# Optimization experiments

Hardware: AMD Instinct MI355X
Metric: run time of the kernel (lower is better)

The kernel has to match this reference:

```python
import jax, jax.numpy as jnp
import numpy as np


def setup_inputs() -> dict:
    key = jax.random.key(0)
    ks = jax.random.split(key, 5)
    B, S, D, H, K = 2, 2048, 1024, 16, 64
    std = 0.02
    return {
        "x": jax.random.normal(ks[0], (B, S, D), dtype=jnp.float32),
        "W_Q": jax.random.normal(ks[1], (H, D, K), dtype=jnp.float32) * std,
        "W_K": jax.random.normal(ks[2], (H, D, K), dtype=jnp.float32) * std,
        "W_V": jax.random.normal(ks[3], (H, D, K), dtype=jnp.float32) * std,
        "W_O": jax.random.normal(ks[4], (H, K, D), dtype=jnp.float32) * std,
        "b_Q": jnp.zeros((H, K), dtype=jnp.float32),
        "b_K": jnp.zeros((H, K), dtype=jnp.float32),
        "b_V": jnp.zeros((H, K), dtype=jnp.float32),
        "b_O": jnp.zeros((D,), dtype=jnp.float32),
    }


def reference(x, W_Q, W_K, W_V, W_O, b_Q, b_K, b_V, b_O):
    # x: (B, S, D); W_*: (H, D, K); W_O: (H, K, D)
    S = x.shape[1]
    d_head = W_Q.shape[-1]
    q = jnp.einsum('bpd,hdk->bphk', x, W_Q) + b_Q
    k = jnp.einsum('bpd,hdk->bphk', x, W_K) + b_K
    v = jnp.einsum('bpd,hdk->bphk', x, W_V) + b_V
    scores = jnp.einsum('bphk,bqhk->bhpq', q, k) / jnp.sqrt(jnp.float32(d_head))
    # causal mask: positions q > p (strict upper triangle) are masked
    causal = jnp.tril(jnp.ones((S, S), dtype=bool))
    scores = jnp.where(causal, scores, jnp.float32(-jnp.inf))
    pattern = jax.nn.softmax(scores, axis=-1)
    z = jnp.einsum('bhpq,bqhk->bphk', pattern, v)
    out = jnp.einsum('bphk,hkd->bpd', z, W_O) + b_O
    return out
```

## Files before the change

### kernel.cpp

```cpp
#include <hip/hip_runtime.h>

typedef unsigned short u16;
typedef __attribute__((ext_vector_type(4))) float f32x4;
typedef __attribute__((ext_vector_type(8))) short s16x8;
typedef __attribute__((ext_vector_type(4))) unsigned short u16x4;
typedef __attribute__((ext_vector_type(2))) unsigned int u32x2;

#define S_ 2048
#define D_ 1024
#define H_ 16
#define KH 64
#define M_ 4096
#define BH_ 32

__device__ __forceinline__ float bf2f(u16 v) {
    union { unsigned int u; float f; } x; x.u = ((unsigned int)v) << 16; return x.f;
}
__device__ __forceinline__ u16 f2bf(float f) {
    union { float ff; unsigned int u; } x; x.ff = f;
    unsigned int r = x.u + 0x7fffu + ((x.u >> 16) & 1u);
    return (u16)(r >> 16);
}
__device__ __forceinline__ unsigned int cvt_pk_bf16(float lo, float hi) {
    unsigned int d;
    asm("v_cvt_pk_bf16_f32 %0, %1, %2" : "=v"(d) : "v"(lo), "v"(hi));
    return d;
}

__global__ void kcvt_x(const float* __restrict__ x, u16* __restrict__ xb) {
    const int i = (blockIdx.x * 256 + threadIdx.x) * 4;
    const float4 v = *(const float4*)&x[i];
    u16x4 o;
    o.x = f2bf(v.x); o.y = f2bf(v.y); o.z = f2bf(v.z); o.w = f2bf(v.w);
    *(u16x4*)&xb[i] = o;
}

__global__ void ktrans_w(const float* __restrict__ WQ, const float* __restrict__ WK,
                         const float* __restrict__ WV, const float* __restrict__ WO,
                         u16* __restrict__ wt) {
    __shared__ u16 tile[64][65];
    const int mat = blockIdx.z;
    const float* src = (mat == 0) ? WQ : (mat == 1) ? WK : (mat == 2) ? WV : WO;
    u16* dst = wt + (size_t)mat * 1048576;
    const int a0 = blockIdx.x * 64, b0 = blockIdx.y * 64;
    const int t = threadIdx.x;
    const int bl = t & 63, ar = t >> 6;
    #pragma unroll
    for (int i = 0; i < 16; ++i) {
        int a = a0 + i * 4 + ar, b = b0 + bl;
        size_t sa = (mat < 3) ? (((size_t)(b >> 6)) << 16) + ((size_t)a << 6) + (b & 63)
                              : (size_t)a * 1024 + b;
        tile[i * 4 + ar][bl] = f2bf(src[sa]);
    }
    __syncthreads();
    #pragma unroll
    for (int i = 0; i < 16; ++i) {
        int bl2 = i * 4 + ar;
        dst[(size_t)(b0 + bl2) * 1024 + a0 + bl] = tile[bl][bl2];
    }
}

__global__ void ktrans_v(const u16* __restrict__ V, u16* __restrict__ Vt) {
    __shared__ u16 tile[64][65];
    const int bh = blockIdx.y;
    const int s0 = blockIdx.x * 64;
    const u16* src = V + (size_t)bh * S_ * KH;
    u16* dst = Vt + (size_t)bh * S_ * KH;
    const int t = threadIdx.x, kl = t & 63, sr = t >> 6;
    #pragma unroll
    for (int i = 0; i < 16; ++i)
        tile[i * 4 + sr][kl] = src[(size_t)(s0 + i * 4 + sr) * KH + kl];
    __syncthreads();
    #pragma unroll
    for (int i = 0; i < 16; ++i) {
        int k = i * 4 + sr;
        dst[(size_t)k * S_ + s0 + kl] = tile[kl][k];
    }
}

template <int MODE>
__global__ __launch_bounds__(256)
void kgemm(const u16* __restrict__ A, const u16* __restrict__ Wt,
           const float* __restrict__ b0p, const float* __restrict__ b1p,
           const float* __restrict__ b2p,
           u16* __restrict__ o0, u16* __restrict__ o1, u16* __restrict__ o2,
           float* __restrict__ fo) {
    __shared__ u16 As[2][128 * 32];
    __shared__ u16 Bs[2][128 * 32];
    const int t = threadIdx.x;
    const int l = t & 63, w = t >> 6;
    const int lq = l & 15, lg = l >> 4;
    const int wr = w >> 1, wc = w & 1;
    const int m0 = blockIdx.x * 128;
    const int n0 = blockIdx.y * 128;

    const u16* Bt;
    const float* bias;
    u16* out = nullptr;
    if constexpr (MODE == 0) {
        const int z = blockIdx.z;
        Bt = Wt + (size_t)z * 1048576;
        bias = (z == 0) ? b0p : (z == 1) ? b1p : b2p;
        out = (z == 0) ? o0 : (z == 1) ? o1 : o2;
    } else {
        Bt = Wt; bias = b0p;
    }

    f32x4 acc[4][4] = {};

    auto stage = [&](int kt, int buf) {
        #pragma unroll
        for (int i = 0; i < 2; ++i) {
            int idx = t + i * 256;
            int row = idx >> 2, cc = idx & 3;
            const u16* ga = A + (size_t)(m0 + row) * 1024 + kt * 32 + cc * 8;
            const u16* gb = Bt + (size_t)(n0 + row) * 1024 + kt * 32 + cc * 8;
            __builtin_amdgcn_global_load_lds(
                (const __attribute__((address_space(1))) unsigned int*)ga,
                (__attribute__((address_space(3))) unsigned int*)(&As[buf][idx * 8]),
                16, 0, 0);
            __builtin_amdgcn_global_load_lds(
                (const __attribute__((address_space(1))) unsigned int*)gb,
                (__attribute__((address_space(3))) unsigned int*)(&Bs[buf][idx * 8]),
                16, 0, 0);
        }
    };

    stage(0, 0);
    __syncthreads();
    for (int kt = 0; kt < 32; ++kt) {
        const int cur = kt & 1;
        if (kt + 1 < 32) stage(kt + 1, cur ^ 1);
        s16x8 af[4], bf[4];
        #pragma unroll
        for (int m = 0; m < 4; ++m)
            af[m] = *(const s16x8*)&As[cur][(wr * 64 + m * 16 + lq) * 32 + lg * 8];
        #pragma unroll
        for (int n = 0; n < 4; ++n)
            bf[n] = *(const s16x8*)&Bs[cur][(wc * 64 + n * 16 + lq) * 32 + lg * 8];
        #pragma unroll
        for (int m = 0; m < 4; ++m)
            #pragma unroll
            for (int n = 0; n < 4; ++n)
                acc[m][n] = __builtin_amdgcn_mfma_f32_16x16x32_bf16(
                    af[m], bf[n], acc[m][n], 0, 0, 0);
        __syncthreads();
    }

    #pragma unroll
    for (int n = 0; n < 4; ++n) {
        const int gcol = n0 + wc * 64 + n * 16 + lq;
        const float bv = bias[gcol];
        #pragma unroll
        for (int m = 0; m < 4; ++m) {
            const int growb = m0 + wr * 64 + m * 16 + lg * 4;
            #pragma unroll
            for (int r = 0; r < 4; ++r) {
                const float v = acc[m][n][r] + bv;
                const int grow = growb + r;
                if constexpr (MODE == 0) {
                    const int b = grow >> 11, s = grow & 2047;
                    const int h = gcol >> 6, kk = gcol & 63;
                    out[(((size_t)(b * H_ + h)) * S_ + s) * KH + kk] = f2bf(v);
                } else {
                    fo[(size_t)grow * 1024 + gcol] = v;
                }
            }
        }
    }
}

__global__ __launch_bounds__(256)
void kattn(const u16* __restrict__ Q, const u16* __restrict__ K,
           const u16* __restrict__ Vt, u16* __restrict__ Z) {
    __shared__ u16 Ks[2][64 * 64];
    __shared__ u16 Vs[2][64 * 64];
    __shared__ u16 Pl[4][16 * 72];
    const int t = threadIdx.x, l = t & 63, w = t >> 6;
    const int lq = l & 15, lg = l >> 4;
    const int bh = blockIdx.y, pair = blockIdx.x;
    const size_t base = (size_t)bh * (S_ * KH);
    const u16* Qb = Q + base;
    const u16* Kb = K + base;
    const u16* Vb = Vt + base;
    const int b = bh >> 4, h = bh & 15;
    u16* Pw = &Pl[w][0];

    const int c0 = ((lg ^ (lq & 7)) * 8);
    const int c1 = c0 ^ 32;
    const float NINF = -__builtin_inff();

    auto stage = [&](int k0, int buf) {
        #pragma unroll
        for (int i = 0; i < 2; ++i) {
            const int idx = t + i * 256;
            const int row = idx >> 3;
            const int cg = (idx & 7) ^ (row & 7);
            __builtin_amdgcn_global_load_lds(
                (const __attribute__((address_space(1))) unsigned int*)
                    (Kb + (size_t)(k0 + row) * KH + cg * 8),
                (__attribute__((address_space(3))) unsigned int*)(&Ks[buf][idx * 8]),
                16, 0, 0);
            __builtin_amdgcn_global_load_lds(
                (const __attribute__((address_space(1))) unsigned int*)
                    (Vb + (size_t)row * S_ + k0 + cg * 8),
                (__attribute__((address_space(3))) unsigned int*)(&Vs[buf][idx * 8]),
                16, 0, 0);
        }
    };

    const float SCL = 0.18033688011112042f;

    #pragma unroll 1
    for (int ph = 0; ph < 2; ++ph) {
        const int qt = ph ? (31 - pair) : pair;
        const int nt = qt + 1;
        const int qs = qt * 64 + w * 16;
        const int lim = w * 16 + lq;

        const s16x8 qf0 = *(const s16x8*)&Qb[(size_t)(qs + lq) * KH + lg * 8];
        const s16x8 qf1 = *(const s16x8*)&Qb[(size_t)(qs + lq) * KH + 32 + lg * 8];

        float mrow = NINF;
        float lrow = 0.f;
        f32x4 zacc[4] = {};

        stage(0, 0);
        __syncthreads();

        for (int kt = 0; kt < nt; ++kt) {
            const int buf = kt & 1;
            if (kt + 1 < nt) stage((kt + 1) * 64, buf ^ 1);

            f32x4 sf[4] = {};
            __builtin_amdgcn_s_setprio(1);
            #pragma unroll
            for (int kf = 0; kf < 4; ++kf) {
                const int row = kf * 16 + lq;
                const s16x8 ka = *(const s16x8*)&Ks[buf][row * 64 + c0];
                const s16x8 kb = *(const s16x8*)&Ks[buf][row * 64 + c1];
                sf[kf] = __builtin_amdgcn_mfma_f32_16x16x32_bf16(ka, qf0, sf[kf], 0, 0, 0);
                sf[kf] = __builtin_amdgcn_mfma_f32_16x16x32_bf16(kb, qf1, sf[kf], 0, 0, 0);
            }
            __builtin_amdgcn_s_setprio(0);

            float p[4][4];
            const bool diag = (kt == qt);
            #pragma unroll
            for (int kf = 0; kf < 4; ++kf)
                #pragma unroll
                for (int r = 0; r < 4; ++r) {
                    float v = sf[kf][r] * SCL;
                    if (diag && (kf * 16 + lg * 4 + r) > lim) v = NINF;
                    p[kf][r] = v;
                }

            float mk[4];
            #pragma unroll
            for (int kf = 0; kf < 4; ++kf)
                mk[kf] = fmaxf(fmaxf(p[kf][0], p[kf][1]), fmaxf(p[kf][2], p[kf][3]));
            float tmax = fmaxf(fmaxf(mk[0], mk[1]), fmaxf(mk[2], mk[3]));
            tmax = fmaxf(tmax, __shfl_xor(tmax, 16));
            tmax = fmaxf(tmax, __shfl_xor(tmax, 32));

            float alpha = 1.f;
            if (!__all(tmax <= mrow + 8.f)) {
                const float nm = fmaxf(mrow, tmax);
                alpha = exp2f(mrow - nm);
                mrow = nm;
                float alp[4];
                #pragma unroll
                for (int r = 0; r < 4; ++r)
                    alp[r] = __shfl(alpha, lg * 4 + r);
                #pragma unroll
                for (int nf = 0; nf < 4; ++nf)
                    #pragma unroll
                    for (int r = 0; r < 4; ++r)
                        zacc[nf][r] *= alp[r];
            }

            float sk[4];
            #pragma unroll
            for (int kf = 0; kf < 4; ++kf) {
                #pragma unroll
                for (int r = 0; r < 4; ++r)
                    p[kf][r] = exp2f(p[kf][r] - mrow);
                sk[kf] = (p[kf][0] + p[kf][1]) + (p[kf][2] + p[kf][3]);
            }
            float rsum = (sk[0] + sk[1]) + (sk[2] + sk[3]);
            rsum += __shfl_xor(rsum, 16);
            rsum += __shfl_xor(rsum, 32);
            lrow = lrow * alpha + rsum;

            #pragma unroll
            for (int kf = 0; kf < 4; ++kf) {
                u32x2 wp;
                wp.x = cvt_pk_bf16(p[kf][0], p[kf][1]);
                wp.y = cvt_pk_bf16(p[kf][2], p[kf][3]);
                *(u32x2*)&Pw[lq * 72 + kf * 16 + lg * 4] = wp;
            }
            const s16x8 pa0 = *(const s16x8*)&Pw[lq * 72 + lg * 8];
            const s16x8 pa1 = *(const s16x8*)&Pw[lq * 72 + 32 + lg * 8];

            __builtin_amdgcn_s_setprio(1);
            #pragma unroll
            for (int nf = 0; nf < 4; ++nf) {
                const int row = nf * 16 + lq;
                const s16x8 v0 = *(const s16x8*)&Vs[buf][row * 64 + c0];
                const s16x8 v1 = *(const s16x8*)&Vs[buf][row * 64 + c1];
                zacc[nf] = __builtin_amdgcn_mfma_f32_16x16x32_bf16(pa0, v0, zacc[nf], 0, 0, 0);
                zacc[nf] = __builtin_amdgcn_mfma_f32_16x16x32_bf16(pa1, v1, zacc[nf], 0, 0, 0);
            }
            __builtin_amdgcn_s_setprio(0);
            __syncthreads();
        }

        float rinv[4];
        #pragma unroll
        for (int r = 0; r < 4; ++r)
            rinv[r] = 1.f / __shfl(lrow, lg * 4 + r);
        #pragma unroll
        for (int nf = 0; nf < 4; ++nf)
            #pragma unroll
            for (int r = 0; r < 4; ++r) {
                const float v = zacc[nf][r] * rinv[r];
                const int srow = qs + lg * 4 + r;
                const int col = h * 64 + nf * 16 + lq;
                Z[(size_t)(b * S_ + srow) * 1024 + col] = f2bf(v);
            }
    }
}

extern "C" void kernel_launch(void* const* d_in, const int* in_sizes, int n_in,
                              void* d_out, int out_size, void* d_ws, size_t ws_size,
                              hipStream_t stream) {
    const float* x  = (const float*)d_in[0];
    const float* WQ = (const float*)d_in[1];
    const float* WK = (const float*)d_in[2];
    const float* WV = (const float*)d_in[3];
    const float* WO = (const float*)d_in[4];
    const float* bQ = (const float*)d_in[5];
    const float* bK = (const float*)d_in[6];
    const float* bV = (const float*)d_in[7];
    const float* bO = (const float*)d_in[8];
    float* out = (float*)d_out;

    u16* ws  = (u16*)d_ws;
    u16* xb  = ws;
    u16* wt  = xb + 4194304u;
    u16* Qb  = wt + 4194304u;
    u16* Kb  = Qb + 4194304u;
    u16* Vtb = Kb + 4194304u;
    u16* Zb  = Vtb + 4194304u;
    u16* Vb  = Zb;

    kcvt_x<<<dim3(4096), 256, 0, stream>>>(x, xb);
    ktrans_w<<<dim3(16, 16, 4), 256, 0, stream>>>(WQ, WK, WV, WO, wt);
    kgemm<0><<<dim3(32, 8, 3), 256, 0, stream>>>(
        xb, wt, bQ, bK, bV, Qb, Kb, Vb, nullptr);
    ktrans_v<<<dim3(32, BH_), 256, 0, stream>>>(Vb, Vtb);
    kattn<<<dim3(16, BH_), 256, 0, stream>>>(Qb, Kb, Vtb, Zb);
    kgemm<1><<<dim3(32, 8, 1), 256, 0, stream>>>(
        Zb, wt + 3u * 1048576u, bO, nullptr, nullptr,
        nullptr, nullptr, nullptr, out);
}
```

Before: 215.3 us.

## Fuse V transpose into QKV GEMM epilogue, vectorize stores, remap attention blocks

The QKV projection GEMM now writes V directly in transposed layout, which removes the separate ktrans_v kernel and its extra read/write pass. The MFMA operand order is swapped in the GEMMs and attention so each lane holds four consecutive columns, allowing packed bf16 and float4 stores and removing the per-row shuffles in the softmax rescale and normalization. The output projection uses 128x64 tiles to launch more blocks. Attention blocks are remapped so that heads are grouped per XCD. The cost is scattered 2-byte stores for V^T in the GEMM epilogue.

```diff
diff --git a/kernel.cpp b/kernel.cpp
--- a/kernel.cpp
+++ b/kernel.cpp
@@ -60,31 +60,11 @@
     }
 }
 
-__global__ void ktrans_v(const u16* __restrict__ V, u16* __restrict__ Vt) {
-    __shared__ u16 tile[64][65];
-    const int bh = blockIdx.y;
-    const int s0 = blockIdx.x * 64;
-    const u16* src = V + (size_t)bh * S_ * KH;
-    u16* dst = Vt + (size_t)bh * S_ * KH;
-    const int t = threadIdx.x, kl = t & 63, sr = t >> 6;
-    #pragma unroll
-    for (int i = 0; i < 16; ++i)
-        tile[i * 4 + sr][kl] = src[(size_t)(s0 + i * 4 + sr) * KH + kl];
-    __syncthreads();
-    #pragma unroll
-    for (int i = 0; i < 16; ++i) {
-        int k = i * 4 + sr;
-        dst[(size_t)k * S_ + s0 + kl] = tile[kl][k];
-    }
-}
-
-template <int MODE>
 __global__ __launch_bounds__(256)
-void kgemm(const u16* __restrict__ A, const u16* __restrict__ Wt,
-           const float* __restrict__ b0p, const float* __restrict__ b1p,
-           const float* __restrict__ b2p,
-           u16* __restrict__ o0, u16* __restrict__ o1, u16* __restrict__ o2,
-           float* __restrict__ fo) {
+void kgemm0(const u16* __restrict__ A, const u16* __restrict__ Wt,
+            const float* __restrict__ b0p, const float* __restrict__ b1p,
+            const float* __restrict__ b2p,
+            u16* __restrict__ Qo, u16* __restrict__ Ko, u16* __restrict__ Vto) {
     __shared__ u16 As[2][128 * 32];
     __shared__ u16 Bs[2][128 * 32];
     const int t = threadIdx.x;
@@ -93,18 +73,9 @@
     const int wr = w >> 1, wc = w & 1;
     const int m0 = blockIdx.x * 128;
     const int n0 = blockIdx.y * 128;
-
-    const u16* Bt;
-    const float* bias;
-    u16* out = nullptr;
-    if constexpr (MODE == 0) {
-        const int z = blockIdx.z;
-        Bt = Wt + (size_t)z * 1048576;
-        bias = (z == 0) ? b0p : (z == 1) ? b1p : b2p;
-        out = (z == 0) ? o0 : (z == 1) ? o1 : o2;
-    } else {
-        Bt = Wt; bias = b0p;
-    }
+    const int z = blockIdx.z;
+    const u16* Bt = Wt + (size_t)z * 1048576;
+    const float* bias = (z == 0) ? b0p : (z == 1) ? b1p : b2p;
 
     f32x4 acc[4][4] = {};
 
@@ -143,29 +114,107 @@
             #pragma unroll
             for (int n = 0; n < 4; ++n)
                 acc[m][n] = __builtin_amdgcn_mfma_f32_16x16x32_bf16(
-                    af[m], bf[n], acc[m][n], 0, 0, 0);
+                    bf[n], af[m], acc[m][n], 0, 0, 0);
         __syncthreads();
     }
 
     #pragma unroll
     for (int n = 0; n < 4; ++n) {
-        const int gcol = n0 + wc * 64 + n * 16 + lq;
-        const float bv = bias[gcol];
+        const int gcolb = n0 + wc * 64 + n * 16 + lg * 4;
+        const float4 bv = *(const float4*)&bias[gcolb];
+        const int h = gcolb >> 6, kk0 = gcolb & 63;
         #pragma unroll
         for (int m = 0; m < 4; ++m) {
-            const int growb = m0 + wr * 64 + m * 16 + lg * 4;
-            #pragma unroll
-            for (int r = 0; r < 4; ++r) {
-                const float v = acc[m][n][r] + bv;
-                const int grow = growb + r;
-                if constexpr (MODE == 0) {
-                    const int b = grow >> 11, s = grow & 2047;
-                    const int h = gcol >> 6, kk = gcol & 63;
-                    out[(((size_t)(b * H_ + h)) * S_ + s) * KH + kk] = f2bf(v);
-                } else {
-                    fo[(size_t)grow * 1024 + gcol] = v;
-                }
-            }
+            const int grow = m0 + wr * 64 + m * 16 + lq;
+            const int b = grow >> 11, s = grow & 2047;
+            const float v0 = acc[m][n][0] + bv.x;
+            const float v1 = acc[m][n][1] + bv.y;
+            const float v2 = acc[m][n][2] + bv.z;
+            const float v3 = acc[m][n][3] + bv.w;
+            if (z == 2) {
+                u16* vb = Vto + ((size_t)((b * 16 + h) * 64 + kk0) * 2048 + s);
+                vb[0] = f2bf(v0); vb[2048] = f2bf(v1);
+                vb[4096] = f2bf(v2); vb[6144] = f2bf(v3);
+            } else {
+                u16* outp = (z == 0) ? Qo : Ko;
+                u32x2 wp;
+                wp.x = cvt_pk_bf16(v0, v1);
+                wp.y = cvt_pk_bf16(v2, v3);
+                *(u32x2*)&outp[((size_t)(b * 16 + h) * 2048 + s) * 64 + kk0] = wp;
+            }
+        }
+    }
+}
+
+__global__ __launch_bounds__(256)
+void kgemm1(const u16* __restrict__ A, const u16* __restrict__ Bt,
+            const float* __restrict__ bias, float* __restrict__ fo) {
+    __shared__ u16 As[2][128 * 32];
+    __shared__ u16 Bs[2][64 * 32];
+    const int t = threadIdx.x;
+    const int l = t & 63, w = t >> 6;
+    const int lq = l & 15, lg = l >> 4;
+    const int wr = w >> 1, wc = w & 1;
+    const int m0 = blockIdx.x * 128;
+    const int n0 = blockIdx.y * 64;
+
+    f32x4 acc[4][2] = {};
+
+    auto stage = [&](int kt, int buf) {
+        #pragma unroll
+        for (int i = 0; i < 2; ++i) {
+            int idx = t + i * 256;
+            int row = idx >> 2, cc = idx & 3;
+            __builtin_amdgcn_global_load_lds(
+                (const __attribute__((address_space(1))) unsigned int*)
+                    (A + (size_t)(m0 + row) * 1024 + kt * 32 + cc * 8),
+                (__attribute__((address_space(3))) unsigned int*)(&As[buf][idx * 8]),
+                16, 0, 0);
+        }
+        {
+            int row = t >> 2, cc = t & 3;
+            __builtin_amdgcn_global_load_lds(
+                (const __attribute__((address_space(1))) unsigned int*)
+                    (Bt + (size_t)(n0 + row) * 1024 + kt * 32 + cc * 8),
+                (__attribute__((address_space(3))) unsigned int*)(&Bs[buf][t * 8]),
+                16, 0, 0);
+        }
+    };
+
+    stage(0, 0);
+    __syncthreads();
+    for (int kt = 0; kt < 32; ++kt) {
+        const int cur = kt & 1;
+        if (kt + 1 < 32) stage(kt + 1, cur ^ 1);
+        s16x8 af[4], bf[2];
+        #pragma unroll
+        for (int m = 0; m < 4; ++m)
+            af[m] = *(const s16x8*)&As[cur][(wr * 64 + m * 16 + lq) * 32 + lg * 8];
+        #pragma unroll
+        for (int n = 0; n < 2; ++n)
+            bf[n] = *(const s16x8*)&Bs[cur][(wc * 32 + n * 16 + lq) * 32 + lg * 8];
+        #pragma unroll
+        for (int m = 0; m < 4; ++m)
+            #pragma unroll
+            for (int n = 0; n < 2; ++n)
+                acc[m][n] = __builtin_amdgcn_mfma_f32_16x16x32_bf16(
+                    bf[n], af[m], acc[m][n], 0, 0, 0);
+        __syncthreads();
+    }
+
+    #pragma unroll
+    for (int n = 0; n < 2; ++n) {
+        const int gcolb = n0 + wc * 32 + n * 16 + lg * 4;
+        const float4 bv = *(const float4*)&bias[gcolb];
+        #pragma unroll
+        for (int m = 0; m < 4; ++m) {
+            const int grow = m0 + wr * 64 + m * 16 + lq;
+            float4 o;
+            o.x = acc[m][n][0] + bv.x;
+            o.y = acc[m][n][1] + bv.y;
+            o.z = acc[m][n][2] + bv.z;
+            o.w = acc[m][n][3] + bv.w;
+            *(float4*)&fo[(size_t)grow * 1024 + gcolb] = o;
         }
     }
 }
@@ -178,7 +227,13 @@
     __shared__ u16 Pl[4][16 * 72];
     const int t = threadIdx.x, l = t & 63, w = t >> 6;
     const int lq = l & 15, lg = l >> 4;
-    const int bh = blockIdx.y, pair = blockIdx.x;
+
+    const int lin = blockIdx.x + 16 * blockIdx.y;
+    const int xcd = lin & 7;
+    const int idx = lin >> 3;
+    const int pair = idx & 15;
+    const int bh = xcd + 8 * (idx >> 4);
+
     const size_t base = (size_t)bh * (S_ * KH);
     const u16* Qb = Q + base;
     const u16* Kb = K + base;
@@ -193,18 +248,18 @@
     auto stage = [&](int k0, int buf) {
         #pragma unroll
         for (int i = 0; i < 2; ++i) {
-            const int idx = t + i * 256;
-            const int row = idx >> 3;
-            const int cg = (idx & 7) ^ (row & 7);
+            const int idx2 = t + i * 256;
+            const int row = idx2 >> 3;
+            const int cg = (idx2 & 7) ^ (row & 7);
             __builtin_amdgcn_global_load_lds(
                 (const __attribute__((address_space(1))) unsigned int*)
                     (Kb + (size_t)(k0 + row) * KH + cg * 8),
-                (__attribute__((address_space(3))) unsigned int*)(&Ks[buf][idx * 8]),
+                (__attribute__((address_space(3))) unsigned int*)(&Ks[buf][idx2 * 8]),
                 16, 0, 0);
             __builtin_amdgcn_global_load_lds(
                 (const __attribute__((address_space(1))) unsigned int*)
                     (Vb + (size_t)row * S_ + k0 + cg * 8),
-                (__attribute__((address_space(3))) unsigned int*)(&Vs[buf][idx * 8]),
+                (__attribute__((address_space(3))) unsigned int*)(&Vs[buf][idx2 * 8]),
                 16, 0, 0);
         }
     };
@@ -221,8 +276,7 @@
         const s16x8 qf0 = *(const s16x8*)&Qb[(size_t)(qs + lq) * KH + lg * 8];
         const s16x8 qf1 = *(const s16x8*)&Qb[(size_t)(qs + lq) * KH + 32 + lg * 8];
 
-        float mrow = NINF;
-        float lrow = 0.f;
+        float mrow = NINF, lrow = 0.f;
         f32x4 zacc[4] = {};
 
         stage(0, 0);
@@ -268,15 +322,11 @@
                 const float nm = fmaxf(mrow, tmax);
                 alpha = exp2f(mrow - nm);
                 mrow = nm;
-                float alp[4];
-                #pragma unroll
-                for (int r = 0; r < 4; ++r)
-                    alp[r] = __shfl(alpha, lg * 4 + r);
                 #pragma unroll
                 for (int nf = 0; nf < 4; ++nf)
                     #pragma unroll
                     for (int r = 0; r < 4; ++r)
-                        zacc[nf][r] *= alp[r];
+                        zacc[nf][r] *= alpha;
             }
 
             float sk[4];
@@ -308,26 +358,22 @@
                 const int row = nf * 16 + lq;
                 const s16x8 v0 = *(const s16x8*)&Vs[buf][row * 64 + c0];
                 const s16x8 v1 = *(const s16x8*)&Vs[buf][row * 64 + c1];
-                zacc[nf] = __builtin_amdgcn_mfma_f32_16x16x32_bf16(pa0, v0, zacc[nf], 0, 0, 0);
-                zacc[nf] = __builtin_amdgcn_mfma_f32_16x16x32_bf16(pa1, v1, zacc[nf], 0, 0, 0);
+                zacc[nf] = __builtin_amdgcn_mfma_f32_16x16x32_bf16(v0, pa0, zacc[nf], 0, 0, 0);
+                zacc[nf] = __builtin_amdgcn_mfma_f32_16x16x32_bf16(v1, pa1, zacc[nf], 0, 0, 0);
             }
             __builtin_amdgcn_s_setprio(0);
             __syncthreads();
         }
 
-        float rinv[4];
-        #pragma unroll
-        for (int r = 0; r < 4; ++r)
-            rinv[r] = 1.f / __shfl(lrow, lg * 4 + r);
-        #pragma unroll
-        for (int nf = 0; nf < 4; ++nf)
-            #pragma unroll
-            for (int r = 0; r < 4; ++r) {
-                const float v = zacc[nf][r] * rinv[r];
-                const int srow = qs + lg * 4 + r;
-                const int col = h * 64 + nf * 16 + lq;
-                Z[(size_t)(b * S_ + srow) * 1024 + col] = f2bf(v);
-            }
+        const float rinv = 1.f / lrow;
+        const size_t zrow = (size_t)(b * S_ + qs + lq) * 1024 + h * 64;
+        #pragma unroll
+        for (int nf = 0; nf < 4; ++nf) {
+            u32x2 wp;
+            wp.x = cvt_pk_bf16(zacc[nf][0] * rinv, zacc[nf][1] * rinv);
+            wp.y = cvt_pk_bf16(zacc[nf][2] * rinv, zacc[nf][3] * rinv);
+            *(u32x2*)&Z[zrow + nf * 16 + lg * 4] = wp;
+        }
     }
 }
 
@@ -352,15 +398,12 @@
     u16* Kb  = Qb + 4194304u;
     u16* Vtb = Kb + 4194304u;
     u16* Zb  = Vtb + 4194304u;
-    u16* Vb  = Zb;
 
     kcvt_x<<<dim3(4096), 256, 0, stream>>>(x, xb);
     ktrans_w<<<dim3(16, 16, 4), 256, 0, stream>>>(WQ, WK, WV, WO, wt);
-    kgemm<0><<<dim3(32, 8, 3), 256, 0, stream>>>(
-        xb, wt, bQ, bK, bV, Qb, Kb, Vb, nullptr);
-    ktrans_v<<<dim3(32, BH_), 256, 0, stream>>>(Vb, Vtb);
+    kgemm0<<<dim3(32, 8, 3), 256, 0, stream>>>(
+        xb, wt, bQ, bK, bV, Qb, Kb, Vtb);
     kattn<<<dim3(16, BH_), 256, 0, stream>>>(Qb, Kb, Vtb, Zb);
-    kgemm<1><<<dim3(32, 8, 1), 256, 0, stream>>>(
-        Zb, wt + 3u * 1048576u, bO, nullptr, nullptr,
-        nullptr, nullptr, nullptr, out);
-}
+    kgemm1<<<dim3(32, 16), 256, 0, stream>>>(
+        Zb, wt + 3u * 1048576u, bO, out);
+}
```

Measured after the change: 206.5 us. -4.1%, faster.
